# Optimization experiments

Hardware: AMD Instinct MI355X
Metric: run time of the kernel (lower is better)

## Reference

```python
import jax, jax.numpy as jnp
import numpy as np

IN_DIM = 784
HIDDEN = 512
STYLE = 128
BATCH = 2048
NUM_LABELS = 10


def setup_inputs() -> dict:
    key = jax.random.key(0)
    k1, k2, k3, k4 = jax.random.split(key, 4)
    x = jax.random.uniform(k1, (BATCH, IN_DIM), dtype=jnp.float32)
    m = jax.random.randint(k2, (BATCH,), 0, NUM_LABELS)
    # Embedding tables, scaled as in the torch __init__ (N(0,1)/fan)
    fc1_table = jax.random.normal(k3, (NUM_LABELS, (IN_DIM + 1) * HIDDEN), dtype=jnp.float32) / ((IN_DIM + 1) * HIDDEN)
    fc2_table = jax.random.normal(k4, (NUM_LABELS, (HIDDEN + 1) * STYLE), dtype=jnp.float32) / ((HIDDEN + 1) * STYLE)
    return {"x": x, "m": m, "fc1_table": fc1_table, "fc2_table": fc2_table}


def reference(x, m, fc1_table, fc2_table):
    B = x.shape[0]
    x = x.reshape(B, -1)  # [B, 784]
    # Per-sample weight matrices gathered by label
    fc1 = fc1_table[m].reshape(B, IN_DIM + 1, HIDDEN)   # [B, 785, H]
    fc1_w, fc1_b = fc1[:, :IN_DIM, :], fc1[:, -1, :]
    h1 = jax.nn.relu(jnp.einsum('bkj,bk->bj', fc1_w, x) + fc1_b)  # [B, H]
    fc2 = fc2_table[m].reshape(B, HIDDEN + 1, STYLE)    # [B, H+1, S]
    fc2_w, fc2_b = fc2[:, :HIDDEN, :], fc2[:, -1, :]
    h2 = jnp.einsum('bkj,bk->bj', fc2_w, h1) + fc2_b    # [B, S]
    return jax.nn.sigmoid(h2)
```

## Files before the change

### kernel.cpp

```cpp
#include <hip/hip_runtime.h>
#include <hip/hip_bf16.h>
#include <math.h>

#define BATCH      2048
#define IN_DIM     784
#define HIDDEN     512
#define STYLE      128
#define NUM_LABELS 10
#define FC1_STRIDE ((IN_DIM + 1) * HIDDEN)
#define FC2_STRIDE ((HIDDEN + 1) * STYLE)
#define KP1        832
#define TB         64
#define BK         64
#define MAX_TILES  48

#define META_NTILES 31
#define META_TILES  32
#define META_PERM   176

#define W1B_OFF  16384ULL
#define W2B_OFF  (W1B_OFF + 10ULL*HIDDEN*KP1*2)
#define H1B_OFF  (W2B_OFF + 10ULL*STYLE*HIDDEN*2)
#define BF16_NEED (H1B_OFF + (size_t)BATCH*HIDDEN*2)

#define W1_KB 26
#define W1_NB 16
#define W2_KB 16
#define W2_NB 4
#define W1_BLOCKS (W1_KB*W1_NB*NUM_LABELS)
#define W2_BLOCKS (W2_KB*W2_NB*NUM_LABELS)

typedef short short8  __attribute__((ext_vector_type(8)));
typedef float float4e __attribute__((ext_vector_type(4)));

__device__ __forceinline__ ushort f2b(float v) {
    __hip_bfloat16 h = __float2bfloat16(v);
    return *reinterpret_cast<ushort*>(&h);
}

__global__ void k_prep(const int* __restrict__ m, const float* __restrict__ fc1t,
                       const float* __restrict__ fc2t, int* __restrict__ meta,
                       ushort* __restrict__ w1b, ushort* __restrict__ w2b) {
    const int tid = threadIdx.x;
    int bid = blockIdx.x;

    __shared__ int cnt[NUM_LABELS], curs[NUM_LABELS], offs[NUM_LABELS + 1];
    __shared__ int permS[BATCH];
    __shared__ float tile[32][33];

    if (bid == 0) {
        if (tid < NUM_LABELS) { cnt[tid] = 0; curs[tid] = 0; }
        __syncthreads();
        for (int b = tid; b < BATCH; b += 256) atomicAdd(&cnt[m[b]], 1);
        __syncthreads();
        if (tid == 0) {
            int off = 0;
            for (int L = 0; L < NUM_LABELS; ++L) { offs[L] = off; off += cnt[L]; }
            offs[NUM_LABELS] = off;
        }
        __syncthreads();
        for (int b = tid; b < BATCH; b += 256) {
            int L = m[b];
            int r = atomicAdd(&curs[L], 1);
            permS[offs[L] + r] = b;
        }
        __syncthreads();
        for (int i = tid; i < BATCH; i += 256) meta[META_PERM + i] = permS[i];
        if (tid == 0) {
            int idx = 0;
            for (int L = 0; L < NUM_LABELS; ++L) {
                int c = cnt[L], off = offs[L];
                for (int t = 0; t < c; t += TB) {
                    meta[META_TILES + idx * 3 + 0] = L;
                    meta[META_TILES + idx * 3 + 1] = off + t;
                    meta[META_TILES + idx * 3 + 2] = min(TB, c - t);
                    ++idx;
                }
            }
            meta[META_NTILES] = idx;
        }
        return;
    }

    bid -= 1;
    const float* src; ushort* dst; int Kvalid, Kpad, N, kb, nb, L; size_t srcL, dstL;
    if (bid < W1_BLOCKS) {
        kb = bid % W1_KB; nb = (bid / W1_KB) % W1_NB; L = bid / (W1_KB * W1_NB);
        src = fc1t; dst = w1b; Kvalid = IN_DIM; Kpad = KP1; N = HIDDEN;
        srcL = FC1_STRIDE; dstL = (size_t)HIDDEN * KP1;
    } else {
        bid -= W1_BLOCKS;
        kb = bid % W2_KB; nb = (bid / W2_KB) % W2_NB; L = bid / (W2_KB * W2_NB);
        src = fc2t; dst = w2b; Kvalid = HIDDEN; Kpad = HIDDEN; N = STYLE;
        srcL = FC2_STRIDE; dstL = (size_t)STYLE * HIDDEN;
    }
    const int tx = tid & 31, ty = tid >> 5;
    const int k0 = kb * 32, n0 = nb * 32;
    for (int r = ty; r < 32; r += 8) {
        int k = k0 + r;
        tile[r][tx] = (k < Kvalid) ? src[(size_t)L * srcL + (size_t)k * N + n0 + tx] : 0.f;
    }
    __syncthreads();
    for (int r = ty; r < 32; r += 8) {
        int n = n0 + r;
        dst[(size_t)L * dstL + (size_t)n * Kpad + k0 + tx] = f2b(tile[tx][r]);
    }
}

__launch_bounds__(256)
__global__ void k_fc1m(const float* __restrict__ x, const ushort* __restrict__ w1b,
                       const float* __restrict__ fc1t, const int* __restrict__ meta,
                       ushort* __restrict__ h1b) {
    const int t = blockIdx.x;
    if (t >= meta[META_NTILES]) return;
    const int L      = meta[META_TILES + 3 * t + 0];
    const int pstart = meta[META_TILES + 3 * t + 1];
    const int nrows  = meta[META_TILES + 3 * t + 2];
    const int col0   = blockIdx.y * 64;
    const ushort* __restrict__ W = w1b + (size_t)L * HIDDEN * KP1 + (size_t)col0 * KP1;

    __shared__ int rows[TB];
    __shared__ __align__(16) ushort As[2][64][72];
    __shared__ __align__(16) ushort Bs[2][64][72];

    const int tid = threadIdx.x;
    if (tid < TB) rows[tid] = (tid < nrows) ? meta[META_PERM + pstart + tid] : -1;
    __syncthreads();

    const int sr = tid >> 2, sc = tid & 3;
    const int lane = tid & 63, wv = tid >> 6;
    const int qd = lane >> 4, ln16 = lane & 15;

    const int arow = rows[sr];
    const float* __restrict__ xr = x + (size_t)(arow < 0 ? 0 : arow) * IN_DIM;
    const uint4* __restrict__ bgp = (const uint4*)(W + (size_t)sr * KP1);

    float4e acc[4] = {};
    float4 a0, a1, a2, a3;
    uint4 b0, b1;

    {
        const int ka = sc * 16;
        a0 = make_float4(0.f,0.f,0.f,0.f); a1 = a0; a2 = a0; a3 = a0;
        if (arow >= 0) {
            if (ka      < IN_DIM) a0 = *(const float4*)(xr + ka);
            if (ka + 4  < IN_DIM) a1 = *(const float4*)(xr + ka + 4);
            if (ka + 8  < IN_DIM) a2 = *(const float4*)(xr + ka + 8);
            if (ka + 12 < IN_DIM) a3 = *(const float4*)(xr + ka + 12);
        }
        b0 = bgp[sc * 2 + 0];
        b1 = bgp[sc * 2 + 1];
        ushort av[16];
        av[0]=f2b(a0.x); av[1]=f2b(a0.y); av[2]=f2b(a0.z); av[3]=f2b(a0.w);
        av[4]=f2b(a1.x); av[5]=f2b(a1.y); av[6]=f2b(a1.z); av[7]=f2b(a1.w);
        av[8]=f2b(a2.x); av[9]=f2b(a2.y); av[10]=f2b(a2.z); av[11]=f2b(a2.w);
        av[12]=f2b(a3.x); av[13]=f2b(a3.y); av[14]=f2b(a3.z); av[15]=f2b(a3.w);
        *(uint4*)&As[0][sr][sc * 16 + 0] = *(const uint4*)&av[0];
        *(uint4*)&As[0][sr][sc * 16 + 8] = *(const uint4*)&av[8];
        *(uint4*)&Bs[0][sr][sc * 16 + 0] = b0;
        *(uint4*)&Bs[0][sr][sc * 16 + 8] = b1;
    }
    {
        const int ka = BK + sc * 16;
        a0 = make_float4(0.f,0.f,0.f,0.f); a1 = a0; a2 = a0; a3 = a0;
        if (arow >= 0) {
            if (ka      < IN_DIM) a0 = *(const float4*)(xr + ka);
            if (ka + 4  < IN_DIM) a1 = *(const float4*)(xr + ka + 4);
            if (ka + 8  < IN_DIM) a2 = *(const float4*)(xr + ka + 8);
            if (ka + 12 < IN_DIM) a3 = *(const float4*)(xr + ka + 12);
        }
        b0 = bgp[(BK >> 3) + sc * 2 + 0];
        b1 = bgp[(BK >> 3) + sc * 2 + 1];
    }

    int p = 0;
    for (int k0 = 0; k0 < KP1; k0 += BK) {
        __syncthreads();
        if (k0 + BK < KP1) {
            ushort av[16];
            av[0]=f2b(a0.x); av[1]=f2b(a0.y); av[2]=f2b(a0.z); av[3]=f2b(a0.w);
            av[4]=f2b(a1.x); av[5]=f2b(a1.y); av[6]=f2b(a1.z); av[7]=f2b(a1.w);
            av[8]=f2b(a2.x); av[9]=f2b(a2.y); av[10]=f2b(a2.z); av[11]=f2b(a2.w);
            av[12]=f2b(a3.x); av[13]=f2b(a3.y); av[14]=f2b(a3.z); av[15]=f2b(a3.w);
            *(uint4*)&As[1-p][sr][sc * 16 + 0] = *(const uint4*)&av[0];
            *(uint4*)&As[1-p][sr][sc * 16 + 8] = *(const uint4*)&av[8];
            *(uint4*)&Bs[1-p][sr][sc * 16 + 0] = b0;
            *(uint4*)&Bs[1-p][sr][sc * 16 + 8] = b1;
        }
        if (k0 + 2*BK < KP1) {
            const int ka = k0 + 2*BK + sc * 16;
            a0 = make_float4(0.f,0.f,0.f,0.f); a1 = a0; a2 = a0; a3 = a0;
            if (arow >= 0) {
                if (ka      < IN_DIM) a0 = *(const float4*)(xr + ka);
                if (ka + 4  < IN_DIM) a1 = *(const float4*)(xr + ka + 4);
                if (ka + 8  < IN_DIM) a2 = *(const float4*)(xr + ka + 8);
                if (ka + 12 < IN_DIM) a3 = *(const float4*)(xr + ka + 12);
            }
            b0 = bgp[((k0 + 2*BK) >> 3) + sc * 2 + 0];
            b1 = bgp[((k0 + 2*BK) >> 3) + sc * 2 + 1];
        }
#pragma unroll
        for (int s = 0; s < 2; ++s) {
            short8 af = *(const short8*)&As[p][wv * 16 + ln16][s * 32 + qd * 8];
#pragma unroll
            for (int nt = 0; nt < 4; ++nt) {
                short8 bf = *(const short8*)&Bs[p][nt * 16 + ln16][s * 32 + qd * 8];
                acc[nt] = __builtin_amdgcn_mfma_f32_16x16x32_bf16(af, bf, acc[nt], 0, 0, 0);
            }
        }
        p ^= 1;
    }

    const float* __restrict__ bias = fc1t + (size_t)L * FC1_STRIDE + (size_t)IN_DIM * HIDDEN + col0;
#pragma unroll
    for (int nt = 0; nt < 4; ++nt) {
        const int c = nt * 16 + ln16;
        const float bs = bias[c];
#pragma unroll
        for (int i = 0; i < 4; ++i) {
            const int r = wv * 16 + qd * 4 + i;
            if (r < nrows)
                h1b[(size_t)(pstart + r) * HIDDEN + col0 + c] = f2b(fmaxf(acc[nt][i] + bs, 0.f));
        }
    }
}

__launch_bounds__(256)
__global__ void k_fc2m(const ushort* __restrict__ h1b, const ushort* __restrict__ w2b,
                       const float* __restrict__ fc2t, const int* __restrict__ meta,
                       float* __restrict__ out) {
    const int t = blockIdx.x;
    if (t >= meta[META_NTILES]) return;
    const int L      = meta[META_TILES + 3 * t + 0];
    const int pstart = meta[META_TILES + 3 * t + 1];
    const int nrows  = meta[META_TILES + 3 * t + 2];
    const int col0   = blockIdx.y * 64;
    const ushort* __restrict__ W = w2b + (size_t)L * STYLE * HIDDEN + (size_t)col0 * HIDDEN;

    __shared__ int rows[TB];
    __shared__ __align__(16) ushort As[2][64][72];
    __shared__ __align__(16) ushort Bs[2][64][72];

    const int tid = threadIdx.x;
    if (tid < TB) rows[tid] = (tid < nrows) ? meta[META_PERM + pstart + tid] : -1;
    __syncthreads();

    const int sr = tid >> 2, sc = tid & 3;
    const int lane = tid & 63, wv = tid >> 6;
    const int qd = lane >> 4, ln16 = lane & 15;

    const bool aval = (sr < nrows);
    const uint4* __restrict__ agp = (const uint4*)(h1b + (size_t)(pstart + (aval ? sr : 0)) * HIDDEN);
    const uint4* __restrict__ bgp = (const uint4*)(W + (size_t)sr * HIDDEN);

    float4e acc[4] = {};
    uint4 a0, a1, b0, b1;

    a0 = make_uint4(0u,0u,0u,0u); a1 = a0;
    if (aval) { a0 = agp[sc * 2 + 0]; a1 = agp[sc * 2 + 1]; }
    b0 = bgp[sc * 2 + 0];
    b1 = bgp[sc * 2 + 1];
    *(uint4*)&As[0][sr][sc * 16 + 0] = a0;
    *(uint4*)&As[0][sr][sc * 16 + 8] = a1;
    *(uint4*)&Bs[0][sr][sc * 16 + 0] = b0;
    *(uint4*)&Bs[0][sr][sc * 16 + 8] = b1;
    {
        const int base = (BK >> 3) + sc * 2;
        a0 = make_uint4(0u,0u,0u,0u); a1 = a0;
        if (aval) { a0 = agp[base]; a1 = agp[base + 1]; }
        b0 = bgp[base];
        b1 = bgp[base + 1];
    }

    int p = 0;
    for (int k0 = 0; k0 < HIDDEN; k0 += BK) {
        __syncthreads();
        if (k0 + BK < HIDDEN) {
            *(uint4*)&As[1-p][sr][sc * 16 + 0] = a0;
            *(uint4*)&As[1-p][sr][sc * 16 + 8] = a1;
            *(uint4*)&Bs[1-p][sr][sc * 16 + 0] = b0;
            *(uint4*)&Bs[1-p][sr][sc * 16 + 8] = b1;
        }
        if (k0 + 2*BK < HIDDEN) {
            const int base = ((k0 + 2*BK) >> 3) + sc * 2;
            a0 = make_uint4(0u,0u,0u,0u); a1 = a0;
            if (aval) { a0 = agp[base]; a1 = agp[base + 1]; }
            b0 = bgp[base];
            b1 = bgp[base + 1];
        }
#pragma unroll
        for (int s = 0; s < 2; ++s) {
            short8 af = *(const short8*)&As[p][wv * 16 + ln16][s * 32 + qd * 8];
#pragma unroll
            for (int nt = 0; nt < 4; ++nt) {
                short8 bf = *(const short8*)&Bs[p][nt * 16 + ln16][s * 32 + qd * 8];
                acc[nt] = __builtin_amdgcn_mfma_f32_16x16x32_bf16(af, bf, acc[nt], 0, 0, 0);
            }
        }
        p ^= 1;
    }

    const float* __restrict__ bias = fc2t + (size_t)L * FC2_STRIDE + (size_t)HIDDEN * STYLE + col0;
#pragma unroll
    for (int nt = 0; nt < 4; ++nt) {
        const int c = nt * 16 + ln16;
        const float bs = bias[c];
#pragma unroll
        for (int i = 0; i < 4; ++i) {
            const int r = wv * 16 + qd * 4 + i;
            if (r < nrows) {
                const int orow = rows[r];
                out[(size_t)orow * STYLE + col0 + c] = 1.f / (1.f + __expf(-(acc[nt][i] + bs)));
            }
        }
    }
}

__launch_bounds__(256)
__global__ void k_naive(const float* __restrict__ x, const int* __restrict__ m,
                        const float* __restrict__ fc1t, const float* __restrict__ fc2t,
                        float* __restrict__ out) {
    __shared__ float xs[IN_DIM];
    __shared__ float h1[HIDDEN];
    const int b = blockIdx.x, tid = threadIdx.x, L = m[b];
    for (int k = tid; k < IN_DIM; k += 256) xs[k] = x[(size_t)b * IN_DIM + k];
    __syncthreads();
    const float* __restrict__ W1 = fc1t + (size_t)L * FC1_STRIDE;
    for (int j = tid; j < HIDDEN; j += 256) {
        float acc = W1[(size_t)IN_DIM * HIDDEN + j];
        for (int k = 0; k < IN_DIM; ++k) acc = fmaf(xs[k], W1[(size_t)k * HIDDEN + j], acc);
        h1[j] = fmaxf(acc, 0.f);
    }
    __syncthreads();
    const float* __restrict__ W2 = fc2t + (size_t)L * FC2_STRIDE;
    for (int j = tid; j < STYLE; j += 256) {
        float acc = W2[(size_t)HIDDEN * STYLE + j];
        for (int k = 0; k < HIDDEN; ++k) acc = fmaf(h1[k], W2[(size_t)k * STYLE + j], acc);
        out[(size_t)b * STYLE + j] = 1.f / (1.f + __expf(-acc));
    }
}

extern "C" void kernel_launch(void* const* d_in, const int* in_sizes, int n_in,
                              void* d_out, int out_size, void* d_ws, size_t ws_size,
                              hipStream_t stream) {
    const float* x    = (const float*)d_in[0];
    const int*   m    = (const int*)d_in[1];
    const float* fc1t = (const float*)d_in[2];
    const float* fc2t = (const float*)d_in[3];
    float* out = (float*)d_out;

    if (ws_size >= BF16_NEED) {
        int*    meta = (int*)d_ws;
        ushort* w1b  = (ushort*)((char*)d_ws + W1B_OFF);
        ushort* w2b  = (ushort*)((char*)d_ws + W2B_OFF);
        ushort* h1b  = (ushort*)((char*)d_ws + H1B_OFF);

        k_prep<<<1 + W1_BLOCKS + W2_BLOCKS, 256, 0, stream>>>(m, fc1t, fc2t, meta, w1b, w2b);
        k_fc1m<<<dim3(MAX_TILES, HIDDEN / 64), 256, 0, stream>>>(x, w1b, fc1t, meta, h1b);
        k_fc2m<<<dim3(MAX_TILES, STYLE / 64), 256, 0, stream>>>(h1b, w2b, fc2t, meta, out);
    } else {
        k_naive<<<BATCH, 256, 0, stream>>>(x, m, fc1t, fc2t, out);
    }
}
```

Before: 101.7 us.

## Fuse prep, fc1 and fc2 into one cooperative persistent kernel with grid syncs

Replaces the three-kernel pipeline with one cooperative kernel. It does label bucketing with wave ballots, converts weights and x to bf16 in a shared job loop, and runs the fc1 and fc2 MFMA tiles as grid-stride jobs separated by grid.sync. The aim is to remove launch gaps and let all blocks share the work evenly, and pre-converting x to bf16 makes the A loads simpler. The cost is grid-wide barriers and a dependence on cooperative launch support, with a fallback to the old kernels if that launch fails.

```diff
diff --git a/kernel.cpp b/kernel.cpp
--- a/kernel.cpp
+++ b/kernel.cpp
@@ -1,6 +1,9 @@
 #include <hip/hip_runtime.h>
 #include <hip/hip_bf16.h>
+#include <hip/hip_cooperative_groups.h>
 #include <math.h>
+
+namespace cg = cooperative_groups;
 
 #define BATCH      2048
 #define IN_DIM     784
@@ -21,6 +24,8 @@
 #define W1B_OFF  16384ULL
 #define W2B_OFF  (W1B_OFF + 10ULL*HIDDEN*KP1*2)
 #define H1B_OFF  (W2B_OFF + 10ULL*STYLE*HIDDEN*2)
+#define XB_OFF   (H1B_OFF + (size_t)BATCH*HIDDEN*2)
+#define WS_NEED  (XB_OFF + (size_t)BATCH*KP1*2)
 #define BF16_NEED (H1B_OFF + (size_t)BATCH*HIDDEN*2)
 
 #define W1_KB 26
@@ -29,13 +34,302 @@
 #define W2_NB 4
 #define W1_BLOCKS (W1_KB*W1_NB*NUM_LABELS)
 #define W2_BLOCKS (W2_KB*W2_NB*NUM_LABELS)
+#define XB_JOBS   832
+#define NJOBS0    (W1_BLOCKS + W2_BLOCKS + XB_JOBS)
 
 typedef short short8  __attribute__((ext_vector_type(8)));
 typedef float float4e __attribute__((ext_vector_type(4)));
+typedef ushort ushort4v __attribute__((ext_vector_type(4)));
 
 __device__ __forceinline__ ushort f2b(float v) {
     __hip_bfloat16 h = __float2bfloat16(v);
     return *reinterpret_cast<ushort*>(&h);
+}
+
+union __align__(16) SMem {
+    float prep_tile[32][33];
+    struct {
+        int chunkCnt[32][NUM_LABELS];
+        int chunkPre[32][NUM_LABELS];
+        int labCnt[NUM_LABELS];
+        int labOff[NUM_LABELS + 1];
+    } mt;
+    struct {
+        int rows[TB];
+        ushort As[2][64][72];
+        ushort Bs[2][64][72];
+    } mm;
+};
+
+__launch_bounds__(256)
+__global__ void k_fused(const float* __restrict__ x, const int* __restrict__ m,
+                        const float* __restrict__ fc1t, const float* __restrict__ fc2t,
+                        float* __restrict__ out,
+                        int* __restrict__ meta, ushort* __restrict__ w1b,
+                        ushort* __restrict__ w2b, ushort* __restrict__ h1b,
+                        ushort* __restrict__ xb) {
+    cg::grid_group grid = cg::this_grid();
+    __shared__ SMem sm;
+    const int tid = threadIdx.x;
+    const int bid = blockIdx.x;
+    const int lane = tid & 63, wv = tid >> 6;
+
+    if (bid == 0) {
+        for (int c = wv; c < 32; c += 4) {
+            int L = m[c * 64 + lane];
+#pragma unroll
+            for (int L0 = 0; L0 < NUM_LABELS; ++L0) {
+                unsigned long long mk = __ballot(L == L0);
+                if (lane == L0) sm.mt.chunkCnt[c][L0] = __popcll(mk);
+            }
+        }
+        __syncthreads();
+        if (tid < NUM_LABELS) {
+            int run = 0;
+            for (int c = 0; c < 32; ++c) { sm.mt.chunkPre[c][tid] = run; run += sm.mt.chunkCnt[c][tid]; }
+            sm.mt.labCnt[tid] = run;
+        }
+        __syncthreads();
+        if (tid == 0) {
+            int off = 0;
+            for (int L = 0; L < NUM_LABELS; ++L) { sm.mt.labOff[L] = off; off += sm.mt.labCnt[L]; }
+            sm.mt.labOff[NUM_LABELS] = off;
+            int idx = 0;
+            for (int L = 0; L < NUM_LABELS; ++L) {
+                int c = sm.mt.labCnt[L], o = sm.mt.labOff[L];
+                for (int t = 0; t < c; t += TB) {
+                    meta[META_TILES + idx * 3 + 0] = L;
+                    meta[META_TILES + idx * 3 + 1] = o + t;
+                    meta[META_TILES + idx * 3 + 2] = min(TB, c - t);
+                    ++idx;
+                }
+            }
+            meta[META_NTILES] = idx;
+        }
+        __syncthreads();
+        for (int c = wv; c < 32; c += 4) {
+            int b = c * 64 + lane;
+            int L = m[b];
+#pragma unroll
+            for (int L0 = 0; L0 < NUM_LABELS; ++L0) {
+                unsigned long long mk = __ballot(L == L0);
+                if (L == L0) {
+                    int r = __popcll(mk & ((1ull << lane) - 1ull));
+                    meta[META_PERM + sm.mt.labOff[L0] + sm.mt.chunkPre[c][L0] + r] = b;
+                }
+            }
+        }
+    } else {
+        const int tx = tid & 31, ty = tid >> 5;
+        for (int j = bid - 1; j < NJOBS0; j += (int)gridDim.x - 1) {
+            if (j < W1_BLOCKS + W2_BLOCKS) {
+                int jj = j;
+                const float* src; ushort* dst; int Kvalid, Kpad, N, kb, nb, L; size_t srcL, dstL;
+                if (jj < W1_BLOCKS) {
+                    kb = jj % W1_KB; nb = (jj / W1_KB) % W1_NB; L = jj / (W1_KB * W1_NB);
+                    src = fc1t; dst = w1b; Kvalid = IN_DIM; Kpad = KP1; N = HIDDEN;
+                    srcL = FC1_STRIDE; dstL = (size_t)HIDDEN * KP1;
+                } else {
+                    jj -= W1_BLOCKS;
+                    kb = jj % W2_KB; nb = (jj / W2_KB) % W2_NB; L = jj / (W2_KB * W2_NB);
+                    src = fc2t; dst = w2b; Kvalid = HIDDEN; Kpad = HIDDEN; N = STYLE;
+                    srcL = FC2_STRIDE; dstL = (size_t)STYLE * HIDDEN;
+                }
+                const int k0 = kb * 32, n0 = nb * 32;
+                for (int r = ty; r < 32; r += 8) {
+                    int k = k0 + r;
+                    sm.prep_tile[r][tx] = (k < Kvalid) ? src[(size_t)L * srcL + (size_t)k * N + n0 + tx] : 0.f;
+                }
+                __syncthreads();
+                for (int r = ty; r < 32; r += 8) {
+                    int n = n0 + r;
+                    dst[(size_t)L * dstL + (size_t)n * Kpad + k0 + tx] = f2b(sm.prep_tile[tx][r]);
+                }
+                __syncthreads();
+            } else {
+                int g0 = (j - W1_BLOCKS - W2_BLOCKS) * 512 + tid * 2;
+#pragma unroll
+                for (int q = 0; q < 2; ++q) {
+                    int g = g0 + q;
+                    int b = g / 208, c4 = g % 208;
+                    float4 v = make_float4(0.f, 0.f, 0.f, 0.f);
+                    if (c4 < 196) v = *(const float4*)(x + (size_t)b * IN_DIM + c4 * 4);
+                    ushort4v o;
+                    o.x = f2b(v.x); o.y = f2b(v.y); o.z = f2b(v.z); o.w = f2b(v.w);
+                    *(ushort4v*)(xb + (size_t)b * KP1 + c4 * 4) = o;
+                }
+            }
+        }
+    }
+
+    __threadfence();
+    grid.sync();
+
+    {
+        const int ntiles = meta[META_NTILES];
+        const int njobs = ntiles * (HIDDEN / 64);
+        const int sr = tid >> 2, sc = tid & 3;
+        const int qd = lane >> 4, ln16 = lane & 15;
+        for (int j = bid; j < njobs; j += (int)gridDim.x) {
+            const int t = j >> 3;
+            const int col0 = (j & 7) * 64;
+            const int L      = meta[META_TILES + 3 * t + 0];
+            const int pstart = meta[META_TILES + 3 * t + 1];
+            const int nrows  = meta[META_TILES + 3 * t + 2];
+            const ushort* __restrict__ W = w1b + (size_t)L * HIDDEN * KP1 + (size_t)col0 * KP1;
+
+            if (tid < TB) sm.mm.rows[tid] = (tid < nrows) ? meta[META_PERM + pstart + tid] : -1;
+            __syncthreads();
+
+            const int arow = sm.mm.rows[sr];
+            const bool aval = (arow >= 0);
+            const uint4* __restrict__ agp = (const uint4*)(xb + (size_t)(aval ? arow : 0) * KP1);
+            const uint4* __restrict__ bgp = (const uint4*)(W + (size_t)sr * KP1);
+
+            float4e acc[4] = {};
+            uint4 a0, a1, b0, b1;
+            a0 = make_uint4(0u, 0u, 0u, 0u); a1 = a0;
+            if (aval) { a0 = agp[sc * 2 + 0]; a1 = agp[sc * 2 + 1]; }
+            b0 = bgp[sc * 2 + 0];
+            b1 = bgp[sc * 2 + 1];
+            *(uint4*)&sm.mm.As[0][sr][sc * 16 + 0] = a0;
+            *(uint4*)&sm.mm.As[0][sr][sc * 16 + 8] = a1;
+            *(uint4*)&sm.mm.Bs[0][sr][sc * 16 + 0] = b0;
+            *(uint4*)&sm.mm.Bs[0][sr][sc * 16 + 8] = b1;
+            {
+                const int base = (BK >> 3) + sc * 2;
+                a0 = make_uint4(0u, 0u, 0u, 0u); a1 = a0;
+                if (aval) { a0 = agp[base]; a1 = agp[base + 1]; }
+                b0 = bgp[base];
+                b1 = bgp[base + 1];
+            }
+            int p = 0;
+            for (int k0 = 0; k0 < KP1; k0 += BK) {
+                __syncthreads();
+                if (k0 + BK < KP1) {
+                    *(uint4*)&sm.mm.As[1 - p][sr][sc * 16 + 0] = a0;
+                    *(uint4*)&sm.mm.As[1 - p][sr][sc * 16 + 8] = a1;
+                    *(uint4*)&sm.mm.Bs[1 - p][sr][sc * 16 + 0] = b0;
+                    *(uint4*)&sm.mm.Bs[1 - p][sr][sc * 16 + 8] = b1;
+                }
+                if (k0 + 2 * BK < KP1) {
+                    const int base = ((k0 + 2 * BK) >> 3) + sc * 2;
+                    a0 = make_uint4(0u, 0u, 0u, 0u); a1 = a0;
+                    if (aval) { a0 = agp[base]; a1 = agp[base + 1]; }
+                    b0 = bgp[base];
+                    b1 = bgp[base + 1];
+                }
+#pragma unroll
+                for (int s = 0; s < 2; ++s) {
+                    short8 af = *(const short8*)&sm.mm.As[p][wv * 16 + ln16][s * 32 + qd * 8];
+#pragma unroll
+                    for (int nt = 0; nt < 4; ++nt) {
+                        short8 bf = *(const short8*)&sm.mm.Bs[p][nt * 16 + ln16][s * 32 + qd * 8];
+                        acc[nt] = __builtin_amdgcn_mfma_f32_16x16x32_bf16(af, bf, acc[nt], 0, 0, 0);
+                    }
+                }
+                p ^= 1;
+            }
+            const float* __restrict__ bias = fc1t + (size_t)L * FC1_STRIDE + (size_t)IN_DIM * HIDDEN + col0;
+#pragma unroll
+            for (int nt = 0; nt < 4; ++nt) {
+                const int c = nt * 16 + ln16;
+                const float bs = bias[c];
+#pragma unroll
+                for (int i = 0; i < 4; ++i) {
+                    const int r = wv * 16 + qd * 4 + i;
+                    if (r < nrows)
+                        h1b[(size_t)(pstart + r) * HIDDEN + col0 + c] = f2b(fmaxf(acc[nt][i] + bs, 0.f));
+                }
+            }
+            __syncthreads();
+        }
+    }
+
+    __threadfence();
+    grid.sync();
+
+    {
+        const int ntiles = meta[META_NTILES];
+        const int njobs = ntiles * (STYLE / 64);
+        const int sr = tid >> 2, sc = tid & 3;
+        const int qd = lane >> 4, ln16 = lane & 15;
+        for (int j = bid; j < njobs; j += (int)gridDim.x) {
+            const int t = j >> 1;
+            const int col0 = (j & 1) * 64;
+            const int L      = meta[META_TILES + 3 * t + 0];
+            const int pstart = meta[META_TILES + 3 * t + 1];
+            const int nrows  = meta[META_TILES + 3 * t + 2];
+            const ushort* __restrict__ W = w2b + (size_t)L * STYLE * HIDDEN + (size_t)col0 * HIDDEN;
+
+            if (tid < TB) sm.mm.rows[tid] = (tid < nrows) ? meta[META_PERM + pstart + tid] : -1;
+            __syncthreads();
+
+            const bool aval = (sr < nrows);
+            const uint4* __restrict__ agp = (const uint4*)(h1b + (size_t)(pstart + (aval ? sr : 0)) * HIDDEN);
+            const uint4* __restrict__ bgp = (const uint4*)(W + (size_t)sr * HIDDEN);
+
+            float4e acc[4] = {};
+            uint4 a0, a1, b0, b1;
+            a0 = make_uint4(0u, 0u, 0u, 0u); a1 = a0;
+            if (aval) { a0 = agp[sc * 2 + 0]; a1 = agp[sc * 2 + 1]; }
+            b0 = bgp[sc * 2 + 0];
+            b1 = bgp[sc * 2 + 1];
+            *(uint4*)&sm.mm.As[0][sr][sc * 16 + 0] = a0;
+            *(uint4*)&sm.mm.As[0][sr][sc * 16 + 8] = a1;
+            *(uint4*)&sm.mm.Bs[0][sr][sc * 16 + 0] = b0;
+            *(uint4*)&sm.mm.Bs[0][sr][sc * 16 + 8] = b1;
+            {
+                const int base = (BK >> 3) + sc * 2;
+                a0 = make_uint4(0u, 0u, 0u, 0u); a1 = a0;
+                if (aval) { a0 = agp[base]; a1 = agp[base + 1]; }
+                b0 = bgp[base];
+                b1 = bgp[base + 1];
+            }
+            int p = 0;
+            for (int k0 = 0; k0 < HIDDEN; k0 += BK) {
+                __syncthreads();
+                if (k0 + BK < HIDDEN) {
+                    *(uint4*)&sm.mm.As[1 - p][sr][sc * 16 + 0] = a0;
+                    *(uint4*)&sm.mm.As[1 - p][sr][sc * 16 + 8] = a1;
+                    *(uint4*)&sm.mm.Bs[1 - p][sr][sc * 16 + 0] = b0;
+                    *(uint4*)&sm.mm.Bs[1 - p][sr][sc * 16 + 8] = b1;
+                }
+                if (k0 + 2 * BK < HIDDEN) {
+                    const int base = ((k0 + 2 * BK) >> 3) + sc * 2;
+                    a0 = make_uint4(0u, 0u, 0u, 0u); a1 = a0;
+                    if (aval) { a0 = agp[base]; a1 = agp[base + 1]; }
+                    b0 = bgp[base];
+                    b1 = bgp[base + 1];
+                }
+#pragma unroll
+                for (int s = 0; s < 2; ++s) {
+                    short8 af = *(const short8*)&sm.mm.As[p][wv * 16 + ln16][s * 32 + qd * 8];
+#pragma unroll
+                    for (int nt = 0; nt < 4; ++nt) {
+                        short8 bf = *(const short8*)&sm.mm.Bs[p][nt * 16 + ln16][s * 32 + qd * 8];
+                        acc[nt] = __builtin_amdgcn_mfma_f32_16x16x32_bf16(af, bf, acc[nt], 0, 0, 0);
+                    }
+                }
+                p ^= 1;
+            }
+            const float* __restrict__ bias = fc2t + (size_t)L * FC2_STRIDE + (size_t)HIDDEN * STYLE + col0;
+#pragma unroll
+            for (int nt = 0; nt < 4; ++nt) {
+                const int c = nt * 16 + ln16;
+                const float bs = bias[c];
+#pragma unroll
+                for (int i = 0; i < 4; ++i) {
+                    const int r = wv * 16 + qd * 4 + i;
+                    if (r < nrows) {
+                        const int orow = sm.mm.rows[r];
+                        out[(size_t)orow * STYLE + col0 + c] = 1.f / (1.f + __expf(-(acc[nt][i] + bs)));
+                    }
+                }
+            }
+            __syncthreads();
+        }
+    }
 }
 
 __global__ void k_prep(const int* __restrict__ m, const float* __restrict__ fc1t,
@@ -349,12 +643,40 @@
     const float* fc2t = (const float*)d_in[3];
     float* out = (float*)d_out;
 
-    if (ws_size >= BF16_NEED) {
+    if (ws_size >= WS_NEED) {
         int*    meta = (int*)d_ws;
         ushort* w1b  = (ushort*)((char*)d_ws + W1B_OFF);
         ushort* w2b  = (ushort*)((char*)d_ws + W2B_OFF);
         ushort* h1b  = (ushort*)((char*)d_ws + H1B_OFF);
-
+        ushort* xb   = (ushort*)((char*)d_ws + XB_OFF);
+
+        static int coopBlocks = -2;
+        if (coopBlocks == -2) {
+            int maxb = 0;
+            if (hipOccupancyMaxActiveBlocksPerMultiprocessor(&maxb, k_fused, 256, 0) == hipSuccess && maxb > 0)
+                coopBlocks = maxb;
+            else
+                coopBlocks = 0;
+            (void)hipGetLastError();
+        }
+        if (coopBlocks > 0) {
+            int grid = coopBlocks * 256;
+            if (grid > 1024) grid = 1024;
+            void* args[10] = { (void*)&x, (void*)&m, (void*)&fc1t, (void*)&fc2t, (void*)&out,
+                               (void*)&meta, (void*)&w1b, (void*)&w2b, (void*)&h1b, (void*)&xb };
+            if (hipLaunchCooperativeKernel(k_fused, dim3(grid), dim3(256), args, 0u, stream) == hipSuccess)
+                return;
+            (void)hipGetLastError();
+            coopBlocks = 0;
+        }
+        k_prep<<<1 + W1_BLOCKS + W2_BLOCKS, 256, 0, stream>>>(m, fc1t, fc2t, meta, w1b, w2b);
+        k_fc1m<<<dim3(MAX_TILES, HIDDEN / 64), 256, 0, stream>>>(x, w1b, fc1t, meta, h1b);
+        k_fc2m<<<dim3(MAX_TILES, STYLE / 64), 256, 0, stream>>>(h1b, w2b, fc2t, meta, out);
+    } else if (ws_size >= BF16_NEED) {
+        int*    meta = (int*)d_ws;
+        ushort* w1b  = (ushort*)((char*)d_ws + W1B_OFF);
+        ushort* w2b  = (ushort*)((char*)d_ws + W2B_OFF);
+        ushort* h1b  = (ushort*)((char*)d_ws + H1B_OFF);
         k_prep<<<1 + W1_BLOCKS + W2_BLOCKS, 256, 0, stream>>>(m, fc1t, fc2t, meta, w1b, w2b);
         k_fc1m<<<dim3(MAX_TILES, HIDDEN / 64), 256, 0, stream>>>(x, w1b, fc1t, meta, h1b);
         k_fc2m<<<dim3(MAX_TILES, STYLE / 64), 256, 0, stream>>>(h1b, w2b, fc2t, meta, out);
```

New measurement: 345.9 us. 240% more time.

## Pre-convert x to padded bf16 in prep kernel and use ballot-based label sort

Applied to the files above, without the earlier changes.

The prep kernel gains extra blocks that convert x into a zero-padded bf16 buffer with row stride KP1. The fc1 GEMM then loads A tiles as raw uint4 bf16 with no per-tile float-to-bf16 conversion or bounds checks. The single-block label bucketing is rewritten to use wave ballots and per-chunk prefix sums instead of shared atomics, writing the permutation straight to global memory. This trades redundant conversion work in fc1 (repeated across 8 column blocks) for one extra pass over x and more workspace.

```diff
diff --git a/kernel.cpp b/kernel.cpp
--- a/kernel.cpp
+++ b/kernel.cpp
@@ -21,7 +21,8 @@
 #define W1B_OFF  16384ULL
 #define W2B_OFF  (W1B_OFF + 10ULL*HIDDEN*KP1*2)
 #define H1B_OFF  (W2B_OFF + 10ULL*STYLE*HIDDEN*2)
-#define BF16_NEED (H1B_OFF + (size_t)BATCH*HIDDEN*2)
+#define XB_OFF   (H1B_OFF + (size_t)BATCH*HIDDEN*2)
+#define WS_NEED  (XB_OFF + (size_t)BATCH*KP1*2)
 
 #define W1_KB 26
 #define W1_NB 16
@@ -29,86 +30,127 @@
 #define W2_NB 4
 #define W1_BLOCKS (W1_KB*W1_NB*NUM_LABELS)
 #define W2_BLOCKS (W2_KB*W2_NB*NUM_LABELS)
+#define XB_JOBS   832
 
 typedef short short8  __attribute__((ext_vector_type(8)));
 typedef float float4e __attribute__((ext_vector_type(4)));
+typedef ushort ushort4v __attribute__((ext_vector_type(4)));
 
 __device__ __forceinline__ ushort f2b(float v) {
     __hip_bfloat16 h = __float2bfloat16(v);
     return *reinterpret_cast<ushort*>(&h);
 }
 
-__global__ void k_prep(const int* __restrict__ m, const float* __restrict__ fc1t,
-                       const float* __restrict__ fc2t, int* __restrict__ meta,
-                       ushort* __restrict__ w1b, ushort* __restrict__ w2b) {
+__global__ void k_prep(const float* __restrict__ x, const int* __restrict__ m,
+                       const float* __restrict__ fc1t, const float* __restrict__ fc2t,
+                       int* __restrict__ meta, ushort* __restrict__ w1b,
+                       ushort* __restrict__ w2b, ushort* __restrict__ xb) {
     const int tid = threadIdx.x;
     int bid = blockIdx.x;
-
-    __shared__ int cnt[NUM_LABELS], curs[NUM_LABELS], offs[NUM_LABELS + 1];
-    __shared__ int permS[BATCH];
-    __shared__ float tile[32][33];
+    const int lane = tid & 63, wv = tid >> 6;
+
+    __shared__ union __align__(16) {
+        float tile[32][33];
+        struct {
+            int chunkCnt[32][NUM_LABELS];
+            int chunkPre[32][NUM_LABELS];
+            int labCnt[NUM_LABELS];
+            int labOff[NUM_LABELS + 1];
+        } mt;
+    } sm;
 
     if (bid == 0) {
-        if (tid < NUM_LABELS) { cnt[tid] = 0; curs[tid] = 0; }
-        __syncthreads();
-        for (int b = tid; b < BATCH; b += 256) atomicAdd(&cnt[m[b]], 1);
+        for (int c = wv; c < 32; c += 4) {
+            int L = m[c * 64 + lane];
+#pragma unroll
+            for (int L0 = 0; L0 < NUM_LABELS; ++L0) {
+                unsigned long long mk = __ballot(L == L0);
+                if (lane == L0) sm.mt.chunkCnt[c][L0] = __popcll(mk);
+            }
+        }
+        __syncthreads();
+        if (tid < NUM_LABELS) {
+            int run = 0;
+            for (int c = 0; c < 32; ++c) { sm.mt.chunkPre[c][tid] = run; run += sm.mt.chunkCnt[c][tid]; }
+            sm.mt.labCnt[tid] = run;
+        }
         __syncthreads();
         if (tid == 0) {
             int off = 0;
-            for (int L = 0; L < NUM_LABELS; ++L) { offs[L] = off; off += cnt[L]; }
-            offs[NUM_LABELS] = off;
-        }
-        __syncthreads();
-        for (int b = tid; b < BATCH; b += 256) {
-            int L = m[b];
-            int r = atomicAdd(&curs[L], 1);
-            permS[offs[L] + r] = b;
-        }
-        __syncthreads();
-        for (int i = tid; i < BATCH; i += 256) meta[META_PERM + i] = permS[i];
-        if (tid == 0) {
+            for (int L = 0; L < NUM_LABELS; ++L) { sm.mt.labOff[L] = off; off += sm.mt.labCnt[L]; }
+            sm.mt.labOff[NUM_LABELS] = off;
             int idx = 0;
             for (int L = 0; L < NUM_LABELS; ++L) {
-                int c = cnt[L], off = offs[L];
+                int c = sm.mt.labCnt[L], o = sm.mt.labOff[L];
                 for (int t = 0; t < c; t += TB) {
                     meta[META_TILES + idx * 3 + 0] = L;
-                    meta[META_TILES + idx * 3 + 1] = off + t;
+                    meta[META_TILES + idx * 3 + 1] = o + t;
                     meta[META_TILES + idx * 3 + 2] = min(TB, c - t);
                     ++idx;
                 }
             }
             meta[META_NTILES] = idx;
         }
+        __syncthreads();
+        for (int c = wv; c < 32; c += 4) {
+            int b = c * 64 + lane;
+            int L = m[b];
+#pragma unroll
+            for (int L0 = 0; L0 < NUM_LABELS; ++L0) {
+                unsigned long long mk = __ballot(L == L0);
+                if (L == L0) {
+                    int r = __popcll(mk & ((1ull << lane) - 1ull));
+                    meta[META_PERM + sm.mt.labOff[L0] + sm.mt.chunkPre[c][L0] + r] = b;
+                }
+            }
+        }
         return;
     }
 
     bid -= 1;
-    const float* src; ushort* dst; int Kvalid, Kpad, N, kb, nb, L; size_t srcL, dstL;
-    if (bid < W1_BLOCKS) {
-        kb = bid % W1_KB; nb = (bid / W1_KB) % W1_NB; L = bid / (W1_KB * W1_NB);
-        src = fc1t; dst = w1b; Kvalid = IN_DIM; Kpad = KP1; N = HIDDEN;
-        srcL = FC1_STRIDE; dstL = (size_t)HIDDEN * KP1;
-    } else {
-        bid -= W1_BLOCKS;
-        kb = bid % W2_KB; nb = (bid / W2_KB) % W2_NB; L = bid / (W2_KB * W2_NB);
-        src = fc2t; dst = w2b; Kvalid = HIDDEN; Kpad = HIDDEN; N = STYLE;
-        srcL = FC2_STRIDE; dstL = (size_t)STYLE * HIDDEN;
-    }
-    const int tx = tid & 31, ty = tid >> 5;
-    const int k0 = kb * 32, n0 = nb * 32;
-    for (int r = ty; r < 32; r += 8) {
-        int k = k0 + r;
-        tile[r][tx] = (k < Kvalid) ? src[(size_t)L * srcL + (size_t)k * N + n0 + tx] : 0.f;
-    }
-    __syncthreads();
-    for (int r = ty; r < 32; r += 8) {
-        int n = n0 + r;
-        dst[(size_t)L * dstL + (size_t)n * Kpad + k0 + tx] = f2b(tile[tx][r]);
+    if (bid < W1_BLOCKS + W2_BLOCKS) {
+        const float* src; ushort* dst; int Kvalid, Kpad, N, kb, nb, L; size_t srcL, dstL;
+        if (bid < W1_BLOCKS) {
+            kb = bid % W1_KB; nb = (bid / W1_KB) % W1_NB; L = bid / (W1_KB * W1_NB);
+            src = fc1t; dst = w1b; Kvalid = IN_DIM; Kpad = KP1; N = HIDDEN;
+            srcL = FC1_STRIDE; dstL = (size_t)HIDDEN * KP1;
+        } else {
+            bid -= W1_BLOCKS;
+            kb = bid % W2_KB; nb = (bid / W2_KB) % W2_NB; L = bid / (W2_KB * W2_NB);
+            src = fc2t; dst = w2b; Kvalid = HIDDEN; Kpad = HIDDEN; N = STYLE;
+            srcL = FC2_STRIDE; dstL = (size_t)STYLE * HIDDEN;
+        }
+        const int tx = tid & 31, ty = tid >> 5;
+        const int k0 = kb * 32, n0 = nb * 32;
+        for (int r = ty; r < 32; r += 8) {
+            int k = k0 + r;
+            sm.tile[r][tx] = (k < Kvalid) ? src[(size_t)L * srcL + (size_t)k * N + n0 + tx] : 0.f;
+        }
+        __syncthreads();
+        for (int r = ty; r < 32; r += 8) {
+            int n = n0 + r;
+            dst[(size_t)L * dstL + (size_t)n * Kpad + k0 + tx] = f2b(sm.tile[tx][r]);
+        }
+        return;
+    }
+
+    {
+        int g0 = (bid - W1_BLOCKS - W2_BLOCKS) * 512 + tid * 2;
+#pragma unroll
+        for (int q = 0; q < 2; ++q) {
+            int g = g0 + q;
+            int b = g / 208, c4 = g % 208;
+            float4 v = make_float4(0.f, 0.f, 0.f, 0.f);
+            if (c4 < 196) v = *(const float4*)(x + (size_t)b * IN_DIM + c4 * 4);
+            ushort4v o;
+            o.x = f2b(v.x); o.y = f2b(v.y); o.z = f2b(v.z); o.w = f2b(v.w);
+            *(ushort4v*)(xb + (size_t)b * KP1 + c4 * 4) = o;
+        }
     }
 }
 
 __launch_bounds__(256)
-__global__ void k_fc1m(const float* __restrict__ x, const ushort* __restrict__ w1b,
+__global__ void k_fc1m(const ushort* __restrict__ xb, const ushort* __restrict__ w1b,
                        const float* __restrict__ fc1t, const int* __restrict__ meta,
                        ushort* __restrict__ h1b) {
     const int t = blockIdx.x;
@@ -132,72 +174,44 @@
     const int qd = lane >> 4, ln16 = lane & 15;
 
     const int arow = rows[sr];
-    const float* __restrict__ xr = x + (size_t)(arow < 0 ? 0 : arow) * IN_DIM;
+    const bool aval = (arow >= 0);
+    const uint4* __restrict__ agp = (const uint4*)(xb + (size_t)(aval ? arow : 0) * KP1);
     const uint4* __restrict__ bgp = (const uint4*)(W + (size_t)sr * KP1);
 
     float4e acc[4] = {};
-    float4 a0, a1, a2, a3;
-    uint4 b0, b1;
-
+    uint4 a0, a1, b0, b1;
+
+    a0 = make_uint4(0u, 0u, 0u, 0u); a1 = a0;
+    if (aval) { a0 = agp[sc * 2 + 0]; a1 = agp[sc * 2 + 1]; }
+    b0 = bgp[sc * 2 + 0];
+    b1 = bgp[sc * 2 + 1];
+    *(uint4*)&As[0][sr][sc * 16 + 0] = a0;
+    *(uint4*)&As[0][sr][sc * 16 + 8] = a1;
+    *(uint4*)&Bs[0][sr][sc * 16 + 0] = b0;
+    *(uint4*)&Bs[0][sr][sc * 16 + 8] = b1;
     {
-        const int ka = sc * 16;
-        a0 = make_float4(0.f,0.f,0.f,0.f); a1 = a0; a2 = a0; a3 = a0;
-        if (arow >= 0) {
-            if (ka      < IN_DIM) a0 = *(const float4*)(xr + ka);
-            if (ka + 4  < IN_DIM) a1 = *(const float4*)(xr + ka + 4);
-            if (ka + 8  < IN_DIM) a2 = *(const float4*)(xr + ka + 8);
-            if (ka + 12 < IN_DIM) a3 = *(const float4*)(xr + ka + 12);
-        }
-        b0 = bgp[sc * 2 + 0];
-        b1 = bgp[sc * 2 + 1];
-        ushort av[16];
-        av[0]=f2b(a0.x); av[1]=f2b(a0.y); av[2]=f2b(a0.z); av[3]=f2b(a0.w);
-        av[4]=f2b(a1.x); av[5]=f2b(a1.y); av[6]=f2b(a1.z); av[7]=f2b(a1.w);
-        av[8]=f2b(a2.x); av[9]=f2b(a2.y); av[10]=f2b(a2.z); av[11]=f2b(a2.w);
-        av[12]=f2b(a3.x); av[13]=f2b(a3.y); av[14]=f2b(a3.z); av[15]=f2b(a3.w);
-        *(uint4*)&As[0][sr][sc * 16 + 0] = *(const uint4*)&av[0];
-        *(uint4*)&As[0][sr][sc * 16 + 8] = *(const uint4*)&av[8];
-        *(uint4*)&Bs[0][sr][sc * 16 + 0] = b0;
-        *(uint4*)&Bs[0][sr][sc * 16 + 8] = b1;
-    }
-    {
-        const int ka = BK + sc * 16;
-        a0 = make_float4(0.f,0.f,0.f,0.f); a1 = a0; a2 = a0; a3 = a0;
-        if (arow >= 0) {
-            if (ka      < IN_DIM) a0 = *(const float4*)(xr + ka);
-            if (ka + 4  < IN_DIM) a1 = *(const float4*)(xr + ka + 4);
-            if (ka + 8  < IN_DIM) a2 = *(const float4*)(xr + ka + 8);
-            if (ka + 12 < IN_DIM) a3 = *(const float4*)(xr + ka + 12);
-        }
-        b0 = bgp[(BK >> 3) + sc * 2 + 0];
-        b1 = bgp[(BK >> 3) + sc * 2 + 1];
+        const int base = (BK >> 3) + sc * 2;
+        a0 = make_uint4(0u, 0u, 0u, 0u); a1 = a0;
+        if (aval) { a0 = agp[base]; a1 = agp[base + 1]; }
+        b0 = bgp[base];
+        b1 = bgp[base + 1];
     }
 
     int p = 0;
     for (int k0 = 0; k0 < KP1; k0 += BK) {
         __syncthreads();
         if (k0 + BK < KP1) {
-            ushort av[16];
-            av[0]=f2b(a0.x); av[1]=f2b(a0.y); av[2]=f2b(a0.z); av[3]=f2b(a0.w);
-            av[4]=f2b(a1.x); av[5]=f2b(a1.y); av[6]=f2b(a1.z); av[7]=f2b(a1.w);
-            av[8]=f2b(a2.x); av[9]=f2b(a2.y); av[10]=f2b(a2.z); av[11]=f2b(a2.w);
-            av[12]=f2b(a3.x); av[13]=f2b(a3.y); av[14]=f2b(a3.z); av[15]=f2b(a3.w);
-            *(uint4*)&As[1-p][sr][sc * 16 + 0] = *(const uint4*)&av[0];
-            *(uint4*)&As[1-p][sr][sc * 16 + 8] = *(const uint4*)&av[8];
-            *(uint4*)&Bs[1-p][sr][sc * 16 + 0] = b0;
-            *(uint4*)&Bs[1-p][sr][sc * 16 + 8] = b1;
-        }
-        if (k0 + 2*BK < KP1) {
-            const int ka = k0 + 2*BK + sc * 16;
-            a0 = make_float4(0.f,0.f,0.f,0.f); a1 = a0; a2 = a0; a3 = a0;
-            if (arow >= 0) {
-                if (ka      < IN_DIM) a0 = *(const float4*)(xr + ka);
-                if (ka + 4  < IN_DIM) a1 = *(const float4*)(xr + ka + 4);
-                if (ka + 8  < IN_DIM) a2 = *(const float4*)(xr + ka + 8);
-                if (ka + 12 < IN_DIM) a3 = *(const float4*)(xr + ka + 12);
-            }
-            b0 = bgp[((k0 + 2*BK) >> 3) + sc * 2 + 0];
-            b1 = bgp[((k0 + 2*BK) >> 3) + sc * 2 + 1];
+            *(uint4*)&As[1 - p][sr][sc * 16 + 0] = a0;
+            *(uint4*)&As[1 - p][sr][sc * 16 + 8] = a1;
+            *(uint4*)&Bs[1 - p][sr][sc * 16 + 0] = b0;
+            *(uint4*)&Bs[1 - p][sr][sc * 16 + 8] = b1;
+        }
+        if (k0 + 2 * BK < KP1) {
+            const int base = ((k0 + 2 * BK) >> 3) + sc * 2;
+            a0 = make_uint4(0u, 0u, 0u, 0u); a1 = a0;
+            if (aval) { a0 = agp[base]; a1 = agp[base + 1]; }
+            b0 = bgp[base];
+            b1 = bgp[base + 1];
         }
 #pragma unroll
         for (int s = 0; s < 2; ++s) {
@@ -349,14 +363,15 @@
     const float* fc2t = (const float*)d_in[3];
     float* out = (float*)d_out;
 
-    if (ws_size >= BF16_NEED) {
+    if (ws_size >= WS_NEED) {
         int*    meta = (int*)d_ws;
         ushort* w1b  = (ushort*)((char*)d_ws + W1B_OFF);
         ushort* w2b  = (ushort*)((char*)d_ws + W2B_OFF);
         ushort* h1b  = (ushort*)((char*)d_ws + H1B_OFF);
-
-        k_prep<<<1 + W1_BLOCKS + W2_BLOCKS, 256, 0, stream>>>(m, fc1t, fc2t, meta, w1b, w2b);
-        k_fc1m<<<dim3(MAX_TILES, HIDDEN / 64), 256, 0, stream>>>(x, w1b, fc1t, meta, h1b);
+        ushort* xb   = (ushort*)((char*)d_ws + XB_OFF);
+
+        k_prep<<<1 + W1_BLOCKS + W2_BLOCKS + XB_JOBS, 256, 0, stream>>>(x, m, fc1t, fc2t, meta, w1b, w2b, xb);
+        k_fc1m<<<dim3(MAX_TILES, HIDDEN / 64), 256, 0, stream>>>(xb, w1b, fc1t, meta, h1b);
         k_fc2m<<<dim3(MAX_TILES, STYLE / 64), 256, 0, stream>>>(h1b, w2b, fc2t, meta, out);
     } else {
         k_naive<<<BATCH, 256, 0, stream>>>(x, m, fc1t, fc2t, out);
```

Result: slower. 105.9 us (+4.1%).
